# Kernel tuning notes

Measured on AMD Instinct MI355X. Metric: run time of the kernel, lower is better.

The kernel has to match this reference:

```python
import jax, jax.numpy as jnp
import numpy as np

BATCH = 512
SEQ = 500          # number of time points; SEQ-1 spline pieces
INPUT_CH = 8       # input (control) channels
HIDDEN = 64        # hidden channels (size of z)
HH = 128           # hidden_hidden channels of the CDE func MLP
OUT = 1            # output channels


def setup_inputs() -> dict:
    key = jax.random.key(0)
    ks = jax.random.split(key, 12)
    shp = (BATCH, SEQ - 1, INPUT_CH)
    times = jnp.linspace(0.0, 1.0, SEQ, dtype=jnp.float32)
    coeff_a = jax.random.normal(ks[0], shp, dtype=jnp.float32)
    coeff_b = jax.random.normal(ks[1], shp, dtype=jnp.float32)
    coeff_two_c = jax.random.normal(ks[2], shp, dtype=jnp.float32)
    coeff_three_d = jax.random.normal(ks[3], shp, dtype=jnp.float32)
    # learned parameters
    init_W = jax.random.normal(ks[4], (INPUT_CH, HIDDEN), dtype=jnp.float32) / np.sqrt(INPUT_CH)
    init_b = jnp.zeros((HIDDEN,), dtype=jnp.float32)
    f_W1 = jax.random.normal(ks[5], (HIDDEN, HH), dtype=jnp.float32) / np.sqrt(HIDDEN)
    f_b1 = jnp.zeros((HH,), dtype=jnp.float32)
    f_W2 = jax.random.normal(ks[6], (HH, HIDDEN * INPUT_CH), dtype=jnp.float32) / np.sqrt(HH)
    f_b2 = jnp.zeros((HIDDEN * INPUT_CH,), dtype=jnp.float32)
    lin_W = jax.random.normal(ks[7], (HIDDEN, OUT), dtype=jnp.float32) / np.sqrt(HIDDEN)
    lin_b = jnp.zeros((OUT,), dtype=jnp.float32)
    return dict(times=times, coeff_a=coeff_a, coeff_b=coeff_b,
                coeff_two_c=coeff_two_c, coeff_three_d=coeff_three_d,
                init_W=init_W, init_b=init_b, f_W1=f_W1, f_b1=f_b1,
                f_W2=f_W2, f_b2=f_b2, lin_W=lin_W, lin_b=lin_b)


def reference(times, coeff_a, coeff_b, coeff_two_c, coeff_three_d,
              init_W, init_b, f_W1, f_b1, f_W2, f_b2, lin_W, lin_b):
    n_pieces = coeff_b.shape[1]

    def _interpret_t(t):
        idx = jnp.clip(jnp.sum(t > times) - 1, 0, n_pieces - 1)
        frac = t - times[idx]
        return frac, idx

    def spline_eval(t):  # NaturalCubicSpline.evaluate -> (B, INPUT_CH)
        frac, idx = _interpret_t(t)
        inner = 0.5 * coeff_two_c[:, idx] + coeff_three_d[:, idx] * frac / 3.0
        inner = coeff_b[:, idx] + inner * frac
        return coeff_a[:, idx] + inner * frac

    def dX_dt(t):  # NaturalCubicSpline.derivative -> (B, INPUT_CH)
        frac, idx = _interpret_t(t)
        inner = coeff_two_c[:, idx] + coeff_three_d[:, idx] * frac
        return coeff_b[:, idx] + inner * frac

    def f(z):  # CDE vector field MLP -> (B, HIDDEN, INPUT_CH)
        h = jax.nn.relu(z @ f_W1 + f_b1)
        v = jnp.tanh(h @ f_W2 + f_b2)
        return v.reshape(z.shape[0], HIDDEN, INPUT_CH)

    def F(t, z):  # VectorField: f(z) @ dX/dt -> (B, HIDDEN)
        return jnp.einsum('bhi,bi->bh', f(z), dX_dt(t))

    # initial state from initial_network applied to X(t0)
    z0 = spline_eval(times[0]) @ init_W + init_b  # (B, HIDDEN)

    @jax.checkpoint
    def rk4_step(z, i):
        t0 = times[i]
        h = times[i + 1] - times[i]
        k1 = F(t0, z)
        k2 = F(t0 + 0.5 * h, z + 0.5 * h * k1)
        k3 = F(t0 + 0.5 * h, z + 0.5 * h * k2)
        k4 = F(t0 + h, z + h * k3)
        z_next = z + (h / 6.0) * (k1 + 2.0 * k2 + 2.0 * k3 + k4)
        return z_next, None

    zT, _ = jax.lax.scan(rk4_step, z0, jnp.arange(SEQ - 1))
    # final linear readout + sigmoid activation
    return jax.nn.sigmoid(zT @ lin_W + lin_b)  # (B, OUT)
```

## Files before the change

### kernel.cpp

```cpp
#include <hip/hip_runtime.h>

#define NPIECE 499
#define SEQN 500

typedef __attribute__((ext_vector_type(8))) short bf16x8;
typedef __attribute__((ext_vector_type(4))) float f32x4;
typedef __attribute__((ext_vector_type(2))) float f32x2;

__device__ inline short f2bf(float x) {
    union { float f; unsigned u; } v; v.f = x;
    unsigned r = v.u + 0x7FFFu + ((v.u >> 16) & 1u);
    return (short)(r >> 16);
}

__device__ inline unsigned cvt_pk(float lo, float hi) {
    unsigned r;
    asm("v_cvt_pk_bf16_f32 %0, %1, %2" : "=v"(r) : "v"(lo), "v"(hi));
    return r;
}

__device__ inline float xor16(float x) {
    return __int_as_float(__builtin_amdgcn_ds_swizzle(__float_as_int(x), 0x401f));
}

__global__ void __launch_bounds__(512, 2)
cde_kernel(const float* __restrict__ times,
           const float* __restrict__ ca,  const float* __restrict__ cb,
           const float* __restrict__ c2c, const float* __restrict__ c3d,
           const float* __restrict__ initW, const float* __restrict__ initb,
           const float* __restrict__ W1,  const float* __restrict__ b1,
           const float* __restrict__ W2,  const float* __restrict__ b2,
           const float* __restrict__ linW, const float* __restrict__ linb,
           float* __restrict__ out)
{
    const int tid  = threadIdx.x;
    const int lane = tid & 63;
    const int wv   = tid >> 6;
    const int g    = lane >> 4;
    const int col  = lane & 15;
    const int g0   = g & 1, g1 = g >> 1;
    const int hi   = lane >> 5;
    const int s0   = blockIdx.x * 16;

    __shared__ __align__(16) float tl[SEQN];
    __shared__ __align__(16) short zflat[8][16][8];
    __shared__ __align__(16) short hflat[16][16][8];
    __shared__ __align__(16) float dxl[2][3][2][16][4];
    __shared__ __align__(16) float zinit[64][16];
    __shared__ __align__(16) float pred[8][16];

    for (int j = tid; j < SEQN; j += 512) tl[j] = times[j];

    bf16x8 a2[4][4];
    f32x4  b2f[4];
#pragma unroll
    for (int tt = 0; tt < 4; ++tt) {
        const int o = 16 * (4 * wv + tt) + col;
#pragma unroll
        for (int kk = 0; kk < 4; ++kk) {
            bf16x8 f;
#pragma unroll
            for (int e = 0; e < 8; ++e)
                f[e] = f2bf(W2[(32 * kk + 8 * g + e) * 512 + o]);
            a2[tt][kk] = f;
        }
#pragma unroll
        for (int r = 0; r < 4; ++r)
            b2f[tt][r] = b2[16 * (4 * wv + tt) + 4 * g + r];
    }
    bf16x8 a1[2];
    f32x4  b1f;
    {
        const int o = 16 * wv + col;
#pragma unroll
        for (int kk = 0; kk < 2; ++kk) {
            bf16x8 f;
#pragma unroll
            for (int e = 0; e < 8; ++e)
                f[e] = f2bf(W1[(32 * kk + 8 * g + 2 * (e & 3) + (e >> 2)) * 128 + o]);
            a1[kk] = f;
        }
#pragma unroll
        for (int r = 0; r < 4; ++r) b1f[r] = b1[16 * wv + 4 * g + r];
    }

    const int colz = col ^ (g & 3);
    const short* zr0 = &zflat[g][colz][0];
    const short* zr1 = &zflat[4 + g][colz][0];
    const short* hr0 = &hflat[g][colz][0];
    const short* hr1 = &hflat[4 + g][colz][0];
    const short* hr2 = &hflat[8 + g][colz][0];
    const short* hr3 = &hflat[12 + g][colz][0];
    short* hwp = &hflat[2 * wv + g1][col ^ ((2 * wv + g1) & 3)][4 * g0];
    short* zwp = &zflat[wv][col ^ (wv & 3)][4 * hi];

    __syncthreads();

#pragma unroll
    for (int v = 0; v < 2; ++v) {
        const int idx = tid * 2 + v, hid = idx >> 4, sm = idx & 15;
        float z = initb[hid];
#pragma unroll
        for (int c = 0; c < 8; ++c)
            z += ca[((size_t)(s0 + sm)) * (NPIECE * 8) + c] * initW[c * 64 + hid];
        zinit[hid][sm] = z;
        zflat[hid >> 3][sm ^ ((hid >> 3) & 3)][4 * (hid & 1) + ((hid & 7) >> 1)] = f2bf(z);
    }
    const int pslot = tid >> 7, prr = tid & 127, psm = prr >> 3, pch = prr & 7;
    const size_t prow = ((size_t)(s0 + psm)) * (NPIECE * 8);
    if (tid < 384) {
        float t0n = tl[0], t1n = tl[1], hn = t1n - t0n; int p; float fr;
        if (pslot == 0)      { p = 0; fr = 0.0f; }
        else if (pslot == 1) { p = 0; fr = (t0n + 0.5f * hn) - t0n; }
        else { float t3 = t0n + hn;
               if (t3 > t1n) { p = 1; fr = t3 - t1n; } else { p = 0; fr = t3 - t0n; } }
        const size_t off = prow + (size_t)p * 8 + pch;
        dxl[0][pslot][pch >> 2][psm][pch & 3] = cb[off] + (c2c[off] + c3d[off] * fr) * fr;
    }
    __syncthreads();

    const bool owner = ((lane & 31) < 16);
    float zreg[4], zs[4];
#pragma unroll
    for (int tt = 0; tt < 4; ++tt) {
        zs[tt] = 0.f;
        zreg[tt] = zinit[8 * wv + 2 * tt + hi][col];
    }

    for (int i = 0; i < NPIECE; ++i) {
        const float hs = tl[i + 1] - tl[i];
        const float hs_half = 0.5f * hs, hs_sixth = hs * (1.0f / 6.0f);
        const int par = i & 1;

        float pb = 0.f, pc = 0.f, pd = 0.f, pfr = 0.f;
        const bool pf = (i + 1 < NPIECE) && (tid < 384);
        if (pf) {
            const int j = i + 1;
            float t0n = tl[j], t1n = tl[j + 1], hn = t1n - t0n; int p; float fr;
            if (pslot == 0)      { p = j - 1; fr = t0n - tl[j - 1]; }
            else if (pslot == 1) { p = j; fr = (t0n + 0.5f * hn) - t0n; }
            else { float t3 = t0n + hn;
                   if (j < NPIECE - 1 && t3 > t1n) { p = j + 1; fr = t3 - t1n; }
                   else                            { p = j;     fr = t3 - t0n; } }
            const size_t off = prow + (size_t)p * 8 + pch;
            pb = cb[off]; pc = c2c[off]; pd = c3d[off]; pfr = fr;
        }

        f32x4 ddr0, ddr1, ddr2;
#pragma unroll
        for (int st = 0; st < 4; ++st) {
            __syncthreads();

            if (st == 0) {
                ddr0 = *(const f32x4*)&dxl[par][0][g0][col][0];
                ddr1 = *(const f32x4*)&dxl[par][1][g0][col][0];
                ddr2 = *(const f32x4*)&dxl[par][2][g0][col][0];
            }
            if (st == 3 && pf)
                dxl[par ^ 1][pslot][pch >> 2][psm][pch & 3] = pb + (pc + pd * pfr) * pfr;

            bf16x8 bz0 = *(const bf16x8*)zr0;
            bf16x8 bz1 = *(const bf16x8*)zr1;
            f32x4 ha;
            ha = __builtin_amdgcn_mfma_f32_16x16x32_bf16(a1[0], bz0, b1f, 0, 0, 0);
            ha = __builtin_amdgcn_mfma_f32_16x16x32_bf16(a1[1], bz1, ha, 0, 0, 0);
            int2 hw;
            hw.x = (int)cvt_pk(fmaxf(ha[0], 0.f), fmaxf(ha[1], 0.f));
            hw.y = (int)cvt_pk(fmaxf(ha[2], 0.f), fmaxf(ha[3], 0.f));
            *(int2*)hwp = hw;
            __syncthreads();

            bf16x8 bh0 = *(const bf16x8*)hr0;
            bf16x8 bh1 = *(const bf16x8*)hr1;
            bf16x8 bh2 = *(const bf16x8*)hr2;
            bf16x8 bh3 = *(const bf16x8*)hr3;
            f32x4 cc[4];
#pragma unroll
            for (int tt = 0; tt < 4; ++tt)
                cc[tt] = __builtin_amdgcn_mfma_f32_16x16x32_bf16(a2[tt][0], bh0, b2f[tt], 0, 0, 0);
#pragma unroll
            for (int tt = 0; tt < 4; ++tt)
                cc[tt] = __builtin_amdgcn_mfma_f32_16x16x32_bf16(a2[tt][1], bh1, cc[tt], 0, 0, 0);
#pragma unroll
            for (int tt = 0; tt < 4; ++tt)
                cc[tt] = __builtin_amdgcn_mfma_f32_16x16x32_bf16(a2[tt][2], bh2, cc[tt], 0, 0, 0);
#pragma unroll
            for (int tt = 0; tt < 4; ++tt)
                cc[tt] = __builtin_amdgcn_mfma_f32_16x16x32_bf16(a2[tt][3], bh3, cc[tt], 0, 0, 0);

            const f32x4 dd = (st == 0) ? ddr0 : ((st == 3) ? ddr2 : ddr1);
            float pt[4];
#pragma unroll
            for (int tt = 0; tt < 4; ++tt) {
                f32x2 s2 = {0.f, 0.f};
#pragma unroll
                for (int r2 = 0; r2 < 2; ++r2) {
                    f32x2 x = { cc[tt][2 * r2], cc[tt][2 * r2 + 1] };
                    f32x2 a = x * 2.8853900817779268f;
                    f32x2 e = { __builtin_amdgcn_exp2f(a.x),
                                __builtin_amdgcn_exp2f(a.y) };
                    e = e + 1.0f;
                    f32x2 rr = { __builtin_amdgcn_rcpf(e.x),
                                 __builtin_amdgcn_rcpf(e.y) };
                    f32x2 th = (-2.0f) * rr + 1.0f;
                    f32x2 d2 = { dd[2 * r2], dd[2 * r2 + 1] };
                    s2 = th * d2 + s2;
                }
                pt[tt] = s2.x + s2.y;
            }
#pragma unroll
            for (int tt = 0; tt < 4; ++tt)
                pt[tt] += xor16(pt[tt]);

            if (owner) {
                float zw[4];
#pragma unroll
                for (int tt = 0; tt < 4; ++tt) {
                    const float k = pt[tt];
                    float zst;
                    if (st == 0)      { zs[tt] = k;                    zst = fmaf(hs_half, k, zreg[tt]); }
                    else if (st == 1) { zs[tt] = fmaf(2.f, k, zs[tt]); zst = fmaf(hs_half, k, zreg[tt]); }
                    else if (st == 2) { zs[tt] = fmaf(2.f, k, zs[tt]); zst = fmaf(hs, k, zreg[tt]); }
                    else              { zs[tt] += k;                   zst = fmaf(hs_sixth, zs[tt], zreg[tt]);
                                        zreg[tt] = zst; }
                    zw[tt] = zst;
                }
                int2 wd;
                wd.x = (int)cvt_pk(zw[0], zw[1]);
                wd.y = (int)cvt_pk(zw[2], zw[3]);
                *(int2*)zwp = wd;
            }
        }
    }

    float p = 0.f;
#pragma unroll
    for (int tt = 0; tt < 4; ++tt) p += zreg[tt] * linW[8 * wv + 2 * tt + hi];
    p += __shfl_xor(p, 32);
    if (lane < 16) pred[wv][col] = p;
    __syncthreads();
    if (tid < 16) {
        float a = linb[0];
#pragma unroll
        for (int w = 0; w < 8; ++w) a += pred[w][tid];
        out[s0 + tid] = 1.0f / (1.0f + __expf(-a));
    }
}

extern "C" void kernel_launch(void* const* d_in, const int* in_sizes, int n_in,
                              void* d_out, int out_size, void* d_ws, size_t ws_size,
                              hipStream_t stream) {
    (void)in_sizes; (void)n_in; (void)d_ws; (void)ws_size; (void)out_size;
    const float* times = (const float*)d_in[0];
    const float* ca    = (const float*)d_in[1];
    const float* cb    = (const float*)d_in[2];
    const float* c2c   = (const float*)d_in[3];
    const float* c3d   = (const float*)d_in[4];
    const float* initW = (const float*)d_in[5];
    const float* initb = (const float*)d_in[6];
    const float* W1    = (const float*)d_in[7];
    const float* b1    = (const float*)d_in[8];
    const float* W2    = (const float*)d_in[9];
    const float* b2    = (const float*)d_in[10];
    const float* linW  = (const float*)d_in[11];
    const float* linb  = (const float*)d_in[12];
    cde_kernel<<<32, 512, 0, stream>>>(times, ca, cb, c2c, c3d, initW, initb,
                                       W1, b1, W2, b2, linW, linb, (float*)d_out);
}
```

Measured before the change: 1.870 ms.

## Process two 16-sample groups per block to amortize barriers and interleave MFMA chains

Each block now handles 32 batch samples as two independent 16-sample groups with separate z/h LDS buffers, and the grid shrinks from 32 to 16 blocks. The two groups' MFMA chains are interleaved so the dependent accumulations have independent work between them, and each barrier and the shared timestep bookkeeping are spread over twice the work. The spline-derivative prefetch is also remapped so all 512 threads take part. In exchange, half as many CUs are used and per-thread register pressure roughly doubles, so the serial per-step latency may grow.

```diff
diff --git a/kernel.cpp b/kernel.cpp
--- a/kernel.cpp
+++ b/kernel.cpp
@@ -40,14 +40,14 @@
     const int col  = lane & 15;
     const int g0   = g & 1, g1 = g >> 1;
     const int hi   = lane >> 5;
-    const int s0   = blockIdx.x * 16;
+    const int s0   = blockIdx.x * 32;
 
     __shared__ __align__(16) float tl[SEQN];
-    __shared__ __align__(16) short zflat[8][16][8];
-    __shared__ __align__(16) short hflat[16][16][8];
-    __shared__ __align__(16) float dxl[2][3][2][16][4];
-    __shared__ __align__(16) float zinit[64][16];
-    __shared__ __align__(16) float pred[8][16];
+    __shared__ __align__(16) short zfA[8][16][8],  zfB[8][16][8];
+    __shared__ __align__(16) short hfA[16][16][8], hfB[16][16][8];
+    __shared__ __align__(16) float dxl[2][3][2][32][4];
+    __shared__ __align__(16) float zinit[64][32];
+    __shared__ __align__(16) float pred[8][32];
 
     for (int j = tid; j < SEQN; j += 512) tl[j] = times[j];
 
@@ -85,161 +85,214 @@
     }
 
     const int colz = col ^ (g & 3);
-    const short* zr0 = &zflat[g][colz][0];
-    const short* zr1 = &zflat[4 + g][colz][0];
-    const short* hr0 = &hflat[g][colz][0];
-    const short* hr1 = &hflat[4 + g][colz][0];
-    const short* hr2 = &hflat[8 + g][colz][0];
-    const short* hr3 = &hflat[12 + g][colz][0];
-    short* hwp = &hflat[2 * wv + g1][col ^ ((2 * wv + g1) & 3)][4 * g0];
-    short* zwp = &zflat[wv][col ^ (wv & 3)][4 * hi];
+    const short* zrA0 = &zfA[g][colz][0];      const short* zrB0 = &zfB[g][colz][0];
+    const short* zrA1 = &zfA[4 + g][colz][0];  const short* zrB1 = &zfB[4 + g][colz][0];
+    const short* hrA0 = &hfA[g][colz][0];      const short* hrB0 = &hfB[g][colz][0];
+    const short* hrA1 = &hfA[4 + g][colz][0];  const short* hrB1 = &hfB[4 + g][colz][0];
+    const short* hrA2 = &hfA[8 + g][colz][0];  const short* hrB2 = &hfB[8 + g][colz][0];
+    const short* hrA3 = &hfA[12 + g][colz][0]; const short* hrB3 = &hfB[12 + g][colz][0];
+    short* hwpA = &hfA[2 * wv + g1][col ^ ((2 * wv + g1) & 3)][4 * g0];
+    short* hwpB = &hfB[2 * wv + g1][col ^ ((2 * wv + g1) & 3)][4 * g0];
+    short* zwpA = &zfA[wv][col ^ (wv & 3)][4 * hi];
+    short* zwpB = &zfB[wv][col ^ (wv & 3)][4 * hi];
 
     __syncthreads();
 
 #pragma unroll
-    for (int v = 0; v < 2; ++v) {
-        const int idx = tid * 2 + v, hid = idx >> 4, sm = idx & 15;
+    for (int v = 0; v < 4; ++v) {
+        const int idx = 4 * tid + v, hid = idx >> 5, sm = idx & 31;
         float z = initb[hid];
 #pragma unroll
         for (int c = 0; c < 8; ++c)
             z += ca[((size_t)(s0 + sm)) * (NPIECE * 8) + c] * initW[c * 64 + hid];
         zinit[hid][sm] = z;
-        zflat[hid >> 3][sm ^ ((hid >> 3) & 3)][4 * (hid & 1) + ((hid & 7) >> 1)] = f2bf(z);
-    }
-    const int pslot = tid >> 7, prr = tid & 127, psm = prr >> 3, pch = prr & 7;
+        const int ch = hid >> 3, sl = 4 * (hid & 1) + ((hid & 7) >> 1);
+        const int pcc = (sm & 15) ^ (ch & 3);
+        if (sm < 16) zfA[ch][pcc][sl] = f2bf(z);
+        else         zfB[ch][pcc][sl] = f2bf(z);
+    }
+    const int pidx = tid & 255, psm = pidx >> 3, pch2 = pidx & 7;
     const size_t prow = ((size_t)(s0 + psm)) * (NPIECE * 8);
-    if (tid < 384) {
-        float t0n = tl[0], t1n = tl[1], hn = t1n - t0n; int p; float fr;
-        if (pslot == 0)      { p = 0; fr = 0.0f; }
-        else if (pslot == 1) { p = 0; fr = (t0n + 0.5f * hn) - t0n; }
-        else { float t3 = t0n + hn;
-               if (t3 > t1n) { p = 1; fr = t3 - t1n; } else { p = 0; fr = t3 - t0n; } }
-        const size_t off = prow + (size_t)p * 8 + pch;
-        dxl[0][pslot][pch >> 2][psm][pch & 3] = cb[off] + (c2c[off] + c3d[off] * fr) * fr;
+    const bool hih = (tid >= 256);
+    {
+        float t0n = tl[0], t1n = tl[1], hn = t1n - t0n;
+        if (!hih) {
+            const size_t off = prow + pch2;
+            dxl[0][0][pch2 >> 2][psm][pch2 & 3] = cb[off];
+        } else {
+            float fr = (t0n + 0.5f * hn) - t0n;
+            size_t off = prow + pch2;
+            dxl[0][1][pch2 >> 2][psm][pch2 & 3] = cb[off] + (c2c[off] + c3d[off] * fr) * fr;
+            float t3 = t0n + hn; int p; float fr2;
+            if (t3 > t1n) { p = 1; fr2 = t3 - t1n; } else { p = 0; fr2 = t3 - t0n; }
+            off = prow + (size_t)p * 8 + pch2;
+            dxl[0][2][pch2 >> 2][psm][pch2 & 3] = cb[off] + (c2c[off] + c3d[off] * fr2) * fr2;
+        }
     }
     __syncthreads();
 
     const bool owner = ((lane & 31) < 16);
-    float zreg[4], zs[4];
-#pragma unroll
-    for (int tt = 0; tt < 4; ++tt) {
-        zs[tt] = 0.f;
-        zreg[tt] = zinit[8 * wv + 2 * tt + hi][col];
-    }
+    float zreg[2][4], zs[2][4];
+#pragma unroll
+    for (int grp = 0; grp < 2; ++grp)
+#pragma unroll
+        for (int tt = 0; tt < 4; ++tt) {
+            zs[grp][tt] = 0.f;
+            zreg[grp][tt] = zinit[8 * wv + 2 * tt + hi][16 * grp + col];
+        }
 
     for (int i = 0; i < NPIECE; ++i) {
         const float hs = tl[i + 1] - tl[i];
         const float hs_half = 0.5f * hs, hs_sixth = hs * (1.0f / 6.0f);
         const int par = i & 1;
 
-        float pb = 0.f, pc = 0.f, pd = 0.f, pfr = 0.f;
-        const bool pf = (i + 1 < NPIECE) && (tid < 384);
+        float pb[2], pcf[2], pd[2], pfr[2];
+        const bool pf = (i + 1 < NPIECE);
         if (pf) {
             const int j = i + 1;
-            float t0n = tl[j], t1n = tl[j + 1], hn = t1n - t0n; int p; float fr;
-            if (pslot == 0)      { p = j - 1; fr = t0n - tl[j - 1]; }
-            else if (pslot == 1) { p = j; fr = (t0n + 0.5f * hn) - t0n; }
-            else { float t3 = t0n + hn;
-                   if (j < NPIECE - 1 && t3 > t1n) { p = j + 1; fr = t3 - t1n; }
-                   else                            { p = j;     fr = t3 - t0n; } }
-            const size_t off = prow + (size_t)p * 8 + pch;
-            pb = cb[off]; pc = c2c[off]; pd = c3d[off]; pfr = fr;
-        }
-
-        f32x4 ddr0, ddr1, ddr2;
+            float t0n = tl[j], t1n = tl[j + 1], hn = t1n - t0n;
+            if (!hih) {
+                pfr[0] = t0n - tl[j - 1];
+                const size_t off = prow + (size_t)(j - 1) * 8 + pch2;
+                pb[0] = cb[off]; pcf[0] = c2c[off]; pd[0] = c3d[off];
+            } else {
+                pfr[0] = (t0n + 0.5f * hn) - t0n;
+                size_t off = prow + (size_t)j * 8 + pch2;
+                pb[0] = cb[off]; pcf[0] = c2c[off]; pd[0] = c3d[off];
+                float t3 = t0n + hn; int p;
+                if (j < NPIECE - 1 && t3 > t1n) { p = j + 1; pfr[1] = t3 - t1n; }
+                else                            { p = j;     pfr[1] = t3 - t0n; }
+                off = prow + (size_t)p * 8 + pch2;
+                pb[1] = cb[off]; pcf[1] = c2c[off]; pd[1] = c3d[off];
+            }
+        }
+
 #pragma unroll
         for (int st = 0; st < 4; ++st) {
+            const int dsel = (st == 0) ? 0 : ((st == 3) ? 2 : 1);
             __syncthreads();
 
-            if (st == 0) {
-                ddr0 = *(const f32x4*)&dxl[par][0][g0][col][0];
-                ddr1 = *(const f32x4*)&dxl[par][1][g0][col][0];
-                ddr2 = *(const f32x4*)&dxl[par][2][g0][col][0];
+            const f32x4 ddA = *(const f32x4*)&dxl[par][dsel][g0][col][0];
+            const f32x4 ddB = *(const f32x4*)&dxl[par][dsel][g0][16 + col][0];
+            if (st == 3 && pf) {
+                if (!hih)
+                    dxl[par ^ 1][0][pch2 >> 2][psm][pch2 & 3] =
+                        pb[0] + (pcf[0] + pd[0] * pfr[0]) * pfr[0];
+                else {
+                    dxl[par ^ 1][1][pch2 >> 2][psm][pch2 & 3] =
+                        pb[0] + (pcf[0] + pd[0] * pfr[0]) * pfr[0];
+                    dxl[par ^ 1][2][pch2 >> 2][psm][pch2 & 3] =
+                        pb[1] + (pcf[1] + pd[1] * pfr[1]) * pfr[1];
+                }
             }
-            if (st == 3 && pf)
-                dxl[par ^ 1][pslot][pch >> 2][psm][pch & 3] = pb + (pc + pd * pfr) * pfr;
-
-            bf16x8 bz0 = *(const bf16x8*)zr0;
-            bf16x8 bz1 = *(const bf16x8*)zr1;
-            f32x4 ha;
-            ha = __builtin_amdgcn_mfma_f32_16x16x32_bf16(a1[0], bz0, b1f, 0, 0, 0);
-            ha = __builtin_amdgcn_mfma_f32_16x16x32_bf16(a1[1], bz1, ha, 0, 0, 0);
-            int2 hw;
-            hw.x = (int)cvt_pk(fmaxf(ha[0], 0.f), fmaxf(ha[1], 0.f));
-            hw.y = (int)cvt_pk(fmaxf(ha[2], 0.f), fmaxf(ha[3], 0.f));
-            *(int2*)hwp = hw;
+
+            bf16x8 bzA0 = *(const bf16x8*)zrA0, bzA1 = *(const bf16x8*)zrA1;
+            bf16x8 bzB0 = *(const bf16x8*)zrB0, bzB1 = *(const bf16x8*)zrB1;
+            f32x4 haA, haB;
+            haA = __builtin_amdgcn_mfma_f32_16x16x32_bf16(a1[0], bzA0, b1f, 0, 0, 0);
+            haB = __builtin_amdgcn_mfma_f32_16x16x32_bf16(a1[0], bzB0, b1f, 0, 0, 0);
+            haA = __builtin_amdgcn_mfma_f32_16x16x32_bf16(a1[1], bzA1, haA, 0, 0, 0);
+            haB = __builtin_amdgcn_mfma_f32_16x16x32_bf16(a1[1], bzB1, haB, 0, 0, 0);
+            int2 hwA, hwB;
+            hwA.x = (int)cvt_pk(fmaxf(haA[0], 0.f), fmaxf(haA[1], 0.f));
+            hwA.y = (int)cvt_pk(fmaxf(haA[2], 0.f), fmaxf(haA[3], 0.f));
+            hwB.x = (int)cvt_pk(fmaxf(haB[0], 0.f), fmaxf(haB[1], 0.f));
+            hwB.y = (int)cvt_pk(fmaxf(haB[2], 0.f), fmaxf(haB[3], 0.f));
+            *(int2*)hwpA = hwA;
+            *(int2*)hwpB = hwB;
             __syncthreads();
 
-            bf16x8 bh0 = *(const bf16x8*)hr0;
-            bf16x8 bh1 = *(const bf16x8*)hr1;
-            bf16x8 bh2 = *(const bf16x8*)hr2;
-            bf16x8 bh3 = *(const bf16x8*)hr3;
-            f32x4 cc[4];
-#pragma unroll
-            for (int tt = 0; tt < 4; ++tt)
-                cc[tt] = __builtin_amdgcn_mfma_f32_16x16x32_bf16(a2[tt][0], bh0, b2f[tt], 0, 0, 0);
-#pragma unroll
-            for (int tt = 0; tt < 4; ++tt)
-                cc[tt] = __builtin_amdgcn_mfma_f32_16x16x32_bf16(a2[tt][1], bh1, cc[tt], 0, 0, 0);
-#pragma unroll
-            for (int tt = 0; tt < 4; ++tt)
-                cc[tt] = __builtin_amdgcn_mfma_f32_16x16x32_bf16(a2[tt][2], bh2, cc[tt], 0, 0, 0);
-#pragma unroll
-            for (int tt = 0; tt < 4; ++tt)
-                cc[tt] = __builtin_amdgcn_mfma_f32_16x16x32_bf16(a2[tt][3], bh3, cc[tt], 0, 0, 0);
-
-            const f32x4 dd = (st == 0) ? ddr0 : ((st == 3) ? ddr2 : ddr1);
-            float pt[4];
-#pragma unroll
-            for (int tt = 0; tt < 4; ++tt) {
-                f32x2 s2 = {0.f, 0.f};
-#pragma unroll
-                for (int r2 = 0; r2 < 2; ++r2) {
-                    f32x2 x = { cc[tt][2 * r2], cc[tt][2 * r2 + 1] };
-                    f32x2 a = x * 2.8853900817779268f;
-                    f32x2 e = { __builtin_amdgcn_exp2f(a.x),
-                                __builtin_amdgcn_exp2f(a.y) };
-                    e = e + 1.0f;
-                    f32x2 rr = { __builtin_amdgcn_rcpf(e.x),
-                                 __builtin_amdgcn_rcpf(e.y) };
-                    f32x2 th = (-2.0f) * rr + 1.0f;
-                    f32x2 d2 = { dd[2 * r2], dd[2 * r2 + 1] };
-                    s2 = th * d2 + s2;
+            bf16x8 bhA0 = *(const bf16x8*)hrA0, bhA1 = *(const bf16x8*)hrA1;
+            bf16x8 bhA2 = *(const bf16x8*)hrA2, bhA3 = *(const bf16x8*)hrA3;
+            bf16x8 bhB0 = *(const bf16x8*)hrB0, bhB1 = *(const bf16x8*)hrB1;
+            bf16x8 bhB2 = *(const bf16x8*)hrB2, bhB3 = *(const bf16x8*)hrB3;
+            f32x4 ccA[4], ccB[4];
+#pragma unroll
+            for (int tt = 0; tt < 4; ++tt)
+                ccA[tt] = __builtin_amdgcn_mfma_f32_16x16x32_bf16(a2[tt][0], bhA0, b2f[tt], 0, 0, 0);
+#pragma unroll
+            for (int tt = 0; tt < 4; ++tt)
+                ccB[tt] = __builtin_amdgcn_mfma_f32_16x16x32_bf16(a2[tt][0], bhB0, b2f[tt], 0, 0, 0);
+#pragma unroll
+            for (int tt = 0; tt < 4; ++tt)
+                ccA[tt] = __builtin_amdgcn_mfma_f32_16x16x32_bf16(a2[tt][1], bhA1, ccA[tt], 0, 0, 0);
+#pragma unroll
+            for (int tt = 0; tt < 4; ++tt)
+                ccB[tt] = __builtin_amdgcn_mfma_f32_16x16x32_bf16(a2[tt][1], bhB1, ccB[tt], 0, 0, 0);
+#pragma unroll
+            for (int tt = 0; tt < 4; ++tt)
+                ccA[tt] = __builtin_amdgcn_mfma_f32_16x16x32_bf16(a2[tt][2], bhA2, ccA[tt], 0, 0, 0);
+#pragma unroll
+            for (int tt = 0; tt < 4; ++tt)
+                ccB[tt] = __builtin_amdgcn_mfma_f32_16x16x32_bf16(a2[tt][2], bhB2, ccB[tt], 0, 0, 0);
+#pragma unroll
+            for (int tt = 0; tt < 4; ++tt)
+                ccA[tt] = __builtin_amdgcn_mfma_f32_16x16x32_bf16(a2[tt][3], bhA3, ccA[tt], 0, 0, 0);
+#pragma unroll
+            for (int tt = 0; tt < 4; ++tt)
+                ccB[tt] = __builtin_amdgcn_mfma_f32_16x16x32_bf16(a2[tt][3], bhB3, ccB[tt], 0, 0, 0);
+
+#pragma unroll
+            for (int grp = 0; grp < 2; ++grp) {
+                const f32x4* cc = grp ? ccB : ccA;
+                const f32x4  dd = grp ? ddB : ddA;
+                float pt[4];
+#pragma unroll
+                for (int tt = 0; tt < 4; ++tt) {
+                    f32x2 s2 = {0.f, 0.f};
+#pragma unroll
+                    for (int r2 = 0; r2 < 2; ++r2) {
+                        f32x2 x = { cc[tt][2 * r2], cc[tt][2 * r2 + 1] };
+                        f32x2 a = x * 2.8853900817779268f;
+                        f32x2 e = { __builtin_amdgcn_exp2f(a.x),
+                                    __builtin_amdgcn_exp2f(a.y) };
+                        e = e + 1.0f;
+                        f32x2 rr = { __builtin_amdgcn_rcpf(e.x),
+                                     __builtin_amdgcn_rcpf(e.y) };
+                        f32x2 th = (-2.0f) * rr + 1.0f;
+                        f32x2 d2 = { dd[2 * r2], dd[2 * r2 + 1] };
+                        s2 = th * d2 + s2;
+                    }
+                    pt[tt] = s2.x + s2.y;
                 }
-                pt[tt] = s2.x + s2.y;
+#pragma unroll
+                for (int tt = 0; tt < 4; ++tt)
+                    pt[tt] += xor16(pt[tt]);
+
+                if (owner) {
+                    float zw[4];
+#pragma unroll
+                    for (int tt = 0; tt < 4; ++tt) {
+                        const float k = pt[tt];
+                        float zst;
+                        if (st == 0)      { zs[grp][tt] = k;                         zst = fmaf(hs_half, k, zreg[grp][tt]); }
+                        else if (st == 1) { zs[grp][tt] = fmaf(2.f, k, zs[grp][tt]); zst = fmaf(hs_half, k, zreg[grp][tt]); }
+                        else if (st == 2) { zs[grp][tt] = fmaf(2.f, k, zs[grp][tt]); zst = fmaf(hs, k, zreg[grp][tt]); }
+                        else              { zs[grp][tt] += k;                        zst = fmaf(hs_sixth, zs[grp][tt], zreg[grp][tt]);
+                                            zreg[grp][tt] = zst; }
+                        zw[tt] = zst;
+                    }
+                    int2 wd;
+                    wd.x = (int)cvt_pk(zw[0], zw[1]);
+                    wd.y = (int)cvt_pk(zw[2], zw[3]);
+                    if (grp == 0) *(int2*)zwpA = wd;
+                    else          *(int2*)zwpB = wd;
+                }
             }
-#pragma unroll
-            for (int tt = 0; tt < 4; ++tt)
-                pt[tt] += xor16(pt[tt]);
-
-            if (owner) {
-                float zw[4];
-#pragma unroll
-                for (int tt = 0; tt < 4; ++tt) {
-                    const float k = pt[tt];
-                    float zst;
-                    if (st == 0)      { zs[tt] = k;                    zst = fmaf(hs_half, k, zreg[tt]); }
-                    else if (st == 1) { zs[tt] = fmaf(2.f, k, zs[tt]); zst = fmaf(hs_half, k, zreg[tt]); }
-                    else if (st == 2) { zs[tt] = fmaf(2.f, k, zs[tt]); zst = fmaf(hs, k, zreg[tt]); }
-                    else              { zs[tt] += k;                   zst = fmaf(hs_sixth, zs[tt], zreg[tt]);
-                                        zreg[tt] = zst; }
-                    zw[tt] = zst;
-                }
-                int2 wd;
-                wd.x = (int)cvt_pk(zw[0], zw[1]);
-                wd.y = (int)cvt_pk(zw[2], zw[3]);
-                *(int2*)zwp = wd;
-            }
-        }
-    }
-
-    float p = 0.f;
-#pragma unroll
-    for (int tt = 0; tt < 4; ++tt) p += zreg[tt] * linW[8 * wv + 2 * tt + hi];
-    p += __shfl_xor(p, 32);
-    if (lane < 16) pred[wv][col] = p;
+        }
+    }
+
+    float pacc[2] = {0.f, 0.f};
+#pragma unroll
+    for (int grp = 0; grp < 2; ++grp) {
+#pragma unroll
+        for (int tt = 0; tt < 4; ++tt)
+            pacc[grp] += zreg[grp][tt] * linW[8 * wv + 2 * tt + hi];
+        pacc[grp] += __shfl_xor(pacc[grp], 32);
+    }
+    if (lane < 16) { pred[wv][col] = pacc[0]; pred[wv][16 + col] = pacc[1]; }
     __syncthreads();
-    if (tid < 16) {
+    if (tid < 32) {
         float a = linb[0];
 #pragma unroll
         for (int w = 0; w < 8; ++w) a += pred[w][tid];
@@ -264,6 +317,6 @@
     const float* b2    = (const float*)d_in[10];
     const float* linW  = (const float*)d_in[11];
     const float* linb  = (const float*)d_in[12];
-    cde_kernel<<<32, 512, 0, stream>>>(times, ca, cb, c2c, c3d, initW, initb,
+    cde_kernel<<<16, 512, 0, stream>>>(times, ca, cb, c2c, c3d, initW, initb,
                                        W1, b1, W2, b2, linW, linb, (float*)d_out);
 }
```

Measured after the change: 3.263 ms. 1.75x slower.
